# Kernel optimization log

Measured on AMD Instinct MI355X. Metric: run time of the kernel, lower is better.

Reference implementation:

```python
import jax, jax.numpy as jnp
import numpy as np

B, SI, ST, C, H, D = 1, 1024, 256, 3072, 24, 128
MLP = 4 * C
EPS = 1e-6
SCALE = 1.0 / float(np.sqrt(D))


def _ln(x):
    m = jnp.mean(x, -1, keepdims=True)
    v = jnp.var(x, -1, keepdims=True)
    return (x - m) / jnp.sqrt(v + EPS)


def _rms(x, w):
    return x * jax.lax.rsqrt(jnp.mean(x * x, -1, keepdims=True) + EPS) * w


def _mod(x, shift, scale):
    # AdaLN modulation: x * (1 + scale) + shift, scale/shift are [B, C]
    return x * (1.0 + scale[:, None, :]) + shift[:, None, :]


def _rot_half(x):
    xr, xi = x[..., 0::2], x[..., 1::2]
    return jnp.stack([-xi, xr], -1).reshape(x.shape)


def _rope(x, cos, sin):
    # x: [B, S, H, D]; cos/sin: [S, D]
    return x * cos[None, :, None, :] + _rot_half(x) * sin[None, :, None, :]


def _forward(img, txt, vec, fc, fs,
             i_mod_w, i_mod_b, i_qkv_w, i_qkv_b, i_qn, i_kn, i_pw, i_pb, i_f1w, i_f1b, i_f2w, i_f2b,
             t_mod_w, t_mod_b, t_qkv_w, t_qkv_b, t_qn, t_kn, t_pw, t_pb, t_f1w, t_f1b, t_f2w, t_f2b):
    sv = jax.nn.silu(vec)
    i_s1, i_c1, i_g1, i_s2, i_c2, i_g2 = jnp.split(sv @ i_mod_w + i_mod_b, 6, -1)
    t_s1, t_c1, t_g1, t_s2, t_c2, t_g2 = jnp.split(sv @ t_mod_w + t_mod_b, 6, -1)

    # img stream: LN -> modulate -> QKV -> qk RMSNorm -> RoPE
    iqkv = (_mod(_ln(img), i_s1, i_c1) @ i_qkv_w + i_qkv_b).reshape(B, SI, 3, H, D)
    iq = _rope(_rms(iqkv[:, :, 0], i_qn), fc, fs)
    ik = _rope(_rms(iqkv[:, :, 1], i_kn), fc, fs)
    iv = iqkv[:, :, 2]

    # txt stream: no RoPE
    tqkv = (_mod(_ln(txt), t_s1, t_c1) @ t_qkv_w + t_qkv_b).reshape(B, ST, 3, H, D)
    tq = _rms(tqkv[:, :, 0], t_qn)
    tk = _rms(tqkv[:, :, 1], t_kn)
    tv = tqkv[:, :, 2]

    q = jnp.concatenate([iq, tq], 1)
    k = jnp.concatenate([ik, tk], 1)
    v = jnp.concatenate([iv, tv], 1)

    logits = jnp.einsum('bqhd,bkhd->bhqk', q, k) * SCALE
    o = jnp.einsum('bhqk,bkhd->bqhd', jax.nn.softmax(logits, -1), v).reshape(B, SI + ST, C)
    ia, ta = o[:, :SI], o[:, SI:]

    img = img + (ia @ i_pw + i_pb) * i_g1[:, None, :]
    h = jax.nn.gelu(_mod(_ln(img), i_s2, i_c2) @ i_f1w + i_f1b, approximate=True)
    img = img + (h @ i_f2w + i_f2b) * i_g2[:, None, :]

    txt = txt + (ta @ t_pw + t_pb) * t_g1[:, None, :]
    h = jax.nn.gelu(_mod(_ln(txt), t_s2, t_c2) @ t_f1w + t_f1b, approximate=True)
    txt = txt + (h @ t_f2w + t_f2b) * t_g2[:, None, :]
    return img, txt


def setup_inputs() -> dict:
    key = jax.random.key(0)
    ki = iter(jax.random.split(key, 32))

    def w(shape, s=0.02):
        return jax.random.normal(next(ki), shape, jnp.float32) * s

    # RoPE tables shaped (img_seq_len, head_dim), interleaved pair layout
    pos = jnp.arange(SI, dtype=jnp.float32)
    inv = 1.0 / (10000.0 ** (jnp.arange(0, D, 2, dtype=jnp.float32) / D))
    ang = pos[:, None] * inv[None, :]
    inp = dict(
        img=jax.random.normal(next(ki), (B, SI, C), jnp.float32),
        txt=jax.random.normal(next(ki), (B, ST, C), jnp.float32),
        vec=jax.random.normal(next(ki), (B, C), jnp.float32),
        freqs_cos=jnp.repeat(jnp.cos(ang), 2, -1),
        freqs_sin=jnp.repeat(jnp.sin(ang), 2, -1),
    )
    for p in ('i', 't'):
        inp[p + '_mod_w'] = w((C, 6 * C)); inp[p + '_mod_b'] = jnp.zeros((6 * C,), jnp.float32)
        inp[p + '_qkv_w'] = w((C, 3 * C)); inp[p + '_qkv_b'] = jnp.zeros((3 * C,), jnp.float32)
        inp[p + '_qn'] = jnp.ones((D,), jnp.float32); inp[p + '_kn'] = jnp.ones((D,), jnp.float32)
        inp[p + '_pw'] = w((C, C)); inp[p + '_pb'] = jnp.zeros((C,), jnp.float32)
        inp[p + '_f1w'] = w((C, MLP)); inp[p + '_f1b'] = jnp.zeros((MLP,), jnp.float32)
        inp[p + '_f2w'] = w((MLP, C)); inp[p + '_f2b'] = jnp.zeros((C,), jnp.float32)
    return inp


def reference(img, txt, vec, freqs_cos, freqs_sin,
              i_mod_w, i_mod_b, i_qkv_w, i_qkv_b, i_qn, i_kn, i_pw, i_pb, i_f1w, i_f1b, i_f2w, i_f2b,
              t_mod_w, t_mod_b, t_qkv_w, t_qkv_b, t_qn, t_kn, t_pw, t_pb, t_f1w, t_f1b, t_f2w, t_f2b):
    return _forward(img, txt, vec, freqs_cos, freqs_sin,
                    i_mod_w, i_mod_b, i_qkv_w, i_qkv_b, i_qn, i_kn, i_pw, i_pb, i_f1w, i_f1b, i_f2w, i_f2b,
                    t_mod_w, t_mod_b, t_qkv_w, t_qkv_b, t_qn, t_kn, t_pw, t_pb, t_f1w, t_f1b, t_f2w, t_f2b)
```

## Files before the change

### kernel.cpp

```cpp
#include <hip/hip_runtime.h>


#define SI 1024
#define ST 256
#define SS 1280
#define CC 3072
#define NH 24
#define DH 128
#define MLPD 12288
#define EPSF 1e-6f
#define SCALEF 0.08838834764831845f

typedef __attribute__((ext_vector_type(4))) float f32x4;
typedef __attribute__((ext_vector_type(8))) __bf16 bf16x8;
typedef unsigned short u16;
typedef unsigned int u32;

__device__ __forceinline__ u16 f2bf(float x) {
    union { float f; u32 u; } v; v.f = x;
    u32 r = v.u + 0x7FFFu + ((v.u >> 16) & 1u);
    return (u16)(r >> 16);
}

__device__ __forceinline__ int gsw(int r) {
    return ((r >> 2) & 7) ^ ((r & 3) << 1);
}

__global__ __launch_bounds__(256) void k_modvec(
    const float* __restrict__ vec,
    const float* __restrict__ wi, const float* __restrict__ bi,
    const float* __restrict__ wt, const float* __restrict__ bt,
    float* __restrict__ mi, float* __restrict__ mt)
{
    __shared__ float sv[CC];
    __shared__ float part[7][128];
    int t = threadIdx.x;
    for (int i = t; i < CC; i += 256) {
        float x = vec[i];
        sv[i] = x / (1.f + __expf(-x));
    }
    __syncthreads();
    int gc = blockIdx.x;
    int strm = gc >= 144;
    const float* W  = strm ? wt : wi;
    const float* Bv = strm ? bt : bi;
    float* out      = strm ? mt : mi;
    int c0 = (gc % 144) * 128 + 4 * (t & 31);
    int g  = t >> 5;
    const float* wp  = W + (size_t)(g * 384) * (6 * CC) + c0;
    const float* svp = sv + g * 384;
    f32x4 acc = {0.f, 0.f, 0.f, 0.f};
    for (int r = 0; r < 384; ++r) {
        f32x4 wr = *(const f32x4*)(wp + (size_t)r * (6 * CC));
        float s = svp[r];
        acc.x += wr.x * s; acc.y += wr.y * s; acc.z += wr.z * s; acc.w += wr.w * s;
    }
    int li = t & 31;
    if (g > 0) *(f32x4*)&part[g - 1][li * 4] = acc;
    __syncthreads();
    if (g == 0) {
#pragma unroll
        for (int i = 0; i < 7; ++i) {
            f32x4 p = *(const f32x4*)&part[i][li * 4];
            acc.x += p.x; acc.y += p.y; acc.z += p.z; acc.w += p.w;
        }
        f32x4 bb = *(const f32x4*)(Bv + c0);
        acc.x += bb.x; acc.y += bb.y; acc.z += bb.z; acc.w += bb.w;
        *(f32x4*)(out + c0) = acc;
    }
}

__global__ __launch_bounds__(256) void k_lnmod(
    const float* __restrict__ x,
    const float* __restrict__ shift, const float* __restrict__ scale,
    u16* __restrict__ out)
{
    int r = blockIdx.x;
    const float* xp = x + (size_t)r * CC;
    u16* op = out + (size_t)r * CC;
    int t = threadIdx.x;
    float4 v[3];
    float s = 0.f, q = 0.f;
#pragma unroll
    for (int j = 0; j < 3; ++j) {
        v[j] = *(const float4*)(xp + j * 1024 + t * 4);
        s += v[j].x + v[j].y + v[j].z + v[j].w;
        q += v[j].x * v[j].x + v[j].y * v[j].y + v[j].z * v[j].z + v[j].w * v[j].w;
    }
#pragma unroll
    for (int m = 32; m; m >>= 1) { s += __shfl_xor(s, m); q += __shfl_xor(q, m); }
    __shared__ float red[8];
    int w = t >> 6;
    if ((t & 63) == 0) { red[w] = s; red[4 + w] = q; }
    __syncthreads();
    s = red[0] + red[1] + red[2] + red[3];
    q = red[4] + red[5] + red[6] + red[7];
    float mean = s * (1.f / CC);
    float var  = q * (1.f / CC) - mean * mean;
    float inv  = rsqrtf(var + EPSF);
#pragma unroll
    for (int j = 0; j < 3; ++j) {
        int c0 = j * 1024 + t * 4;
        float4 sh = *(const float4*)(shift + c0);
        float4 sc = *(const float4*)(scale + c0);
        ushort4 o;
        o.x = f2bf((v[j].x - mean) * inv * (1.f + sc.x) + sh.x);
        o.y = f2bf((v[j].y - mean) * inv * (1.f + sc.y) + sh.y);
        o.z = f2bf((v[j].z - mean) * inv * (1.f + sc.z) + sh.z);
        o.w = f2bf((v[j].w - mean) * inv * (1.f + sc.w) + sh.w);
        *(ushort4*)(op + c0) = o;
    }
}

template <int V, int BN>
__global__ __launch_bounds__(512, 2) void k_gemm(
    const u16* __restrict__ A,
    const float* __restrict__ Wi, const float* __restrict__ Wt,
    const float* __restrict__ bi, const float* __restrict__ bt,
    void* __restrict__ outv, int MBI, int N, int K, int lda)
{
    constexpr int BM  = 256;
    constexpr int NWN = (BN == 256) ? 4 : 2;
    constexpr int WM  = (BN == 256) ? 128 : 64;
    constexpr int MI  = WM / 16;
    constexpr int NFB = (BN == 256) ? 8 : 4;

    __shared__ u16 lA[2][BM * 64];
    __shared__ u16 lB[2][BN * 64];
    int t = threadIdx.x;
    int m0 = blockIdx.y * BM;
    int n0 = blockIdx.x * BN;
    bool txts = (blockIdx.y >= (unsigned)MBI);
    const float* W = txts ? Wt : Wi;
    const size_t koff = (size_t)blockIdx.z * K;

    int w = __builtin_amdgcn_readfirstlane(t >> 6);
    int lane = t & 63;
    int wm = (w / NWN) * WM, wn = (w % NWN) * 64;
    int lr = lane & 15, lg = lane >> 4;

    f32x4 acc[MI][4];
#pragma unroll
    for (int i = 0; i < MI; ++i)
#pragma unroll
        for (int j = 0; j < 4; ++j) acc[i][j] = (f32x4){0.f, 0.f, 0.f, 0.f};

    const int bn4 = (BN == 256) ? 4 * (t & 63) : 4 * (t & 31);
    const int bk  = (BN == 256) ? 8 * w : 4 * (t >> 5);
    f32x4 fb[NFB];
    const int NT = K >> 6;

    const float* bptr = W + (koff + bk) * (size_t)N + n0 + bn4;
    const int arow = t >> 3;
    const int acsw = ((t & 7) ^ gsw(arow)) * 8;
    const u16* aptr = A + (size_t)(m0 + arow) * lda + koff + acsw;

    auto LOADB = [&]() {
#pragma unroll
        for (int i = 0; i < NFB; ++i)
            fb[i] = *(const f32x4*)(bptr + (size_t)i * N);
        bptr += (size_t)64 * N;
    };
    auto GLDSA = [&](int buf) {
#pragma unroll
        for (int i = 0; i < 4; ++i) {
            const u16* gp = aptr + (size_t)(i * 64) * lda;
            u16* lp = &lA[buf][(i * 512 + t) * 8];
            __builtin_amdgcn_global_load_lds(
                (const __attribute__((address_space(1))) void*)gp,
                (__attribute__((address_space(3))) void*)lp, 16, 0, 0);
        }
        aptr += 64;
    };
    auto CVTWR = [&](int buf) {
        if constexpr (BN == 256) {
#pragma unroll
            for (int j = 0; j < 4; ++j) {
                int n = bn4 + j;
                union { uint4 q; __bf16 h[8]; } u;
#pragma unroll
                for (int i = 0; i < 8; ++i) u.h[i] = (__bf16)fb[i][j];
                int cp = (bk >> 3) ^ gsw(n);
                *(uint4*)&lB[buf][n * 64 + cp * 8] = u.q;
            }
        } else {
#pragma unroll
            for (int j = 0; j < 4; ++j) {
                int n = bn4 + j;
                union { uint2 q; __bf16 h[4]; } u;
#pragma unroll
                for (int i = 0; i < 4; ++i) u.h[i] = (__bf16)fb[i][j];
                int cp = (bk >> 3) ^ gsw(n);
                *(uint2*)&lB[buf][n * 64 + cp * 8 + (bk & 4)] = u.q;
            }
        }
    };
    auto MFMAP = [&](int buf) {
#pragma unroll
        for (int ks = 0; ks < 2; ++ks) {
            bf16x8 bv[4];
#pragma unroll
            for (int j = 0; j < 4; ++j) {
                int n = wn + j * 16 + lr;
                bv[j] = *(const bf16x8*)&lB[buf][n * 64 + (((ks * 4 + lg) ^ gsw(n)) * 8)];
            }
#pragma unroll
            for (int mh = 0; mh < MI / 4; ++mh) {
                bf16x8 af[4];
#pragma unroll
                for (int i2 = 0; i2 < 4; ++i2) {
                    int m = wm + (mh * 4 + i2) * 16 + lr;
                    af[i2] = *(const bf16x8*)&lA[buf][m * 64 + (((ks * 4 + lg) ^ gsw(m)) * 8)];
                }
                __builtin_amdgcn_s_setprio(1);
#pragma unroll
                for (int i2 = 0; i2 < 4; ++i2)
#pragma unroll
                    for (int j = 0; j < 4; ++j)
                        acc[mh * 4 + i2][j] = __builtin_amdgcn_mfma_f32_16x16x32_bf16(
                            af[i2], bv[j], acc[mh * 4 + i2][j], 0, 0, 0);
                __builtin_amdgcn_s_setprio(0);
            }
        }
    };
    auto VMWN = [&]() {
        if constexpr (BN == 256)
            asm volatile("s_waitcnt vmcnt(8) lgkmcnt(0)" ::: "memory");
        else
            asm volatile("s_waitcnt vmcnt(4) lgkmcnt(0)" ::: "memory");
    };

    LOADB();
    GLDSA(0);
    CVTWR(0);
    if (NT > 1) LOADB();
    VMWN();
    __builtin_amdgcn_s_barrier();
    __builtin_amdgcn_sched_barrier(0);

    int cur = 0;
    for (int kt = 0; kt < NT; ++kt) {
        bool s1 = kt + 1 < NT;
        bool s2 = kt + 2 < NT;
        if (s1) {
            GLDSA(cur ^ 1);
            CVTWR(cur ^ 1);
        }
        if (s2) LOADB();
        MFMAP(cur);
        if (s1) {
            if (s2) { VMWN(); }
            else    { asm volatile("s_waitcnt vmcnt(0) lgkmcnt(0)" ::: "memory"); }
            __builtin_amdgcn_s_barrier();
            __builtin_amdgcn_sched_barrier(0);
        }
        cur ^= 1;
    }

    const float* Bb = txts ? bt : bi;
    int MT = gridDim.y * BM;
#pragma unroll
    for (int i = 0; i < MI; ++i) {
#pragma unroll
        for (int j = 0; j < 4; ++j) {
            int col = n0 + wn + j * 16 + lr;
            float bvv = (V == 3) ? 0.f : Bb[col];
#pragma unroll
            for (int e = 0; e < 4; ++e) {
                int row = m0 + wm + i * 16 + lg * 4 + e;
                float val = acc[i][j][e] + bvv;
                if (V == 0) {
                    ((float*)outv)[(size_t)row * N + col] = val;
                } else if (V == 1) {
                    float g = 0.5f * val * (1.f + tanhf(0.7978845608028654f * (val + 0.044715f * val * val * val)));
                    ((u16*)outv)[(size_t)row * N + col] = f2bf(g);
                } else {
                    ((float*)outv)[((size_t)blockIdx.z * MT + row) * N + col] = val;
                }
            }
        }
    }
}

__global__ __launch_bounds__(256) void k_red(
    const float* __restrict__ p,
    const float* __restrict__ bi, const float* __restrict__ bt,
    const float* __restrict__ gi, const float* __restrict__ gt,
    const float* __restrict__ basei, const float* __restrict__ baset,
    float* __restrict__ out)
{
    int idx4 = blockIdx.x * 256 + threadIdx.x;
    size_t idx = (size_t)idx4 * 4;
    const size_t MN = (size_t)SS * CC;
    int r = idx4 / 768;
    int c = (idx4 - r * 768) * 4;
    bool ts = r >= SI;
    float4 v0 = *(const float4*)(p + idx);
    float4 v1 = *(const float4*)(p + MN + idx);
    float4 bb = *(const float4*)((ts ? bt : bi) + c);
    float4 gg = *(const float4*)((ts ? gt : gi) + c);
    const float* bp = ts ? (baset + (size_t)(r - SI) * CC + c) : (basei + (size_t)r * CC + c);
    float4 ba = *(const float4*)bp;
    float4 o;
    o.x = ba.x + (v0.x + v1.x + bb.x) * gg.x;
    o.y = ba.y + (v0.y + v1.y + bb.y) * gg.y;
    o.z = ba.z + (v0.z + v1.z + bb.z) * gg.z;
    o.w = ba.w + (v0.w + v1.w + bb.w) * gg.w;
    *(float4*)(out + idx) = o;
}

__global__ __launch_bounds__(256) void k_redln(
    const float* __restrict__ p,
    const float* __restrict__ bi, const float* __restrict__ bt,
    const float* __restrict__ gi, const float* __restrict__ gt,
    const float* __restrict__ basei, const float* __restrict__ baset,
    const float* __restrict__ shi, const float* __restrict__ sci,
    const float* __restrict__ sht, const float* __restrict__ sct,
    float* __restrict__ out, u16* __restrict__ xm)
{
    int r = blockIdx.x;
    int t = threadIdx.x;
    bool ts = r >= SI;
    const size_t MN = (size_t)SS * CC;
    const float* b  = ts ? bt : bi;
    const float* g  = ts ? gt : gi;
    const float* base = ts ? (baset + (size_t)(r - SI) * CC) : (basei + (size_t)r * CC);
    const float* p0 = p + (size_t)r * CC;
    const float* p1 = p0 + MN;
    float* op = out + (size_t)r * CC;
    u16*   xp = xm + (size_t)r * CC;

    float4 v[3];
    float s = 0.f, q = 0.f;
#pragma unroll
    for (int j = 0; j < 3; ++j) {
        int c0 = j * 1024 + t * 4;
        float4 a0 = *(const float4*)(p0 + c0);
        float4 a1 = *(const float4*)(p1 + c0);
        float4 bb = *(const float4*)(b + c0);
        float4 gg = *(const float4*)(g + c0);
        float4 ba = *(const float4*)(base + c0);
        float4 o;
        o.x = ba.x + (a0.x + a1.x + bb.x) * gg.x;
        o.y = ba.y + (a0.y + a1.y + bb.y) * gg.y;
        o.z = ba.z + (a0.z + a1.z + bb.z) * gg.z;
        o.w = ba.w + (a0.w + a1.w + bb.w) * gg.w;
        *(float4*)(op + c0) = o;
        v[j] = o;
        s += o.x + o.y + o.z + o.w;
        q += o.x * o.x + o.y * o.y + o.z * o.z + o.w * o.w;
    }
#pragma unroll
    for (int m = 32; m; m >>= 1) { s += __shfl_xor(s, m); q += __shfl_xor(q, m); }
    __shared__ float red[8];
    int w = t >> 6;
    if ((t & 63) == 0) { red[w] = s; red[4 + w] = q; }
    __syncthreads();
    s = red[0] + red[1] + red[2] + red[3];
    q = red[4] + red[5] + red[6] + red[7];
    float mean = s * (1.f / CC);
    float var  = q * (1.f / CC) - mean * mean;
    float inv  = rsqrtf(var + EPSF);
    const float* sh = ts ? sht : shi;
    const float* sc = ts ? sct : sci;
#pragma unroll
    for (int j = 0; j < 3; ++j) {
        int c0 = j * 1024 + t * 4;
        float4 shv = *(const float4*)(sh + c0);
        float4 scv = *(const float4*)(sc + c0);
        ushort4 o;
        o.x = f2bf((v[j].x - mean) * inv * (1.f + scv.x) + shv.x);
        o.y = f2bf((v[j].y - mean) * inv * (1.f + scv.y) + shv.y);
        o.z = f2bf((v[j].z - mean) * inv * (1.f + scv.z) + shv.z);
        o.w = f2bf((v[j].w - mean) * inv * (1.f + scv.w) + shv.w);
        *(ushort4*)(xp + c0) = o;
    }
}

__global__ __launch_bounds__(256) void k_pack(
    const float* __restrict__ qkv,
    const float* __restrict__ iqn, const float* __restrict__ ikn,
    const float* __restrict__ tqn, const float* __restrict__ tkn,
    const float* __restrict__ fc, const float* __restrict__ fs,
    u16* __restrict__ qpk, u16* __restrict__ kpk, u16* __restrict__ vpk)
{
    int wid = blockIdx.x * 4 + (threadIdx.x >> 6);
    int lane = threadIdx.x & 63;
    int s = wid / 72;
    int wh = wid % 72;
    int which = wh / 24;
    int h = wh % 24;
    int d = lane * 2;
    const float* src = qkv + (size_t)s * 9216 + which * 3072 + h * 128 + d;
    float x0 = src[0], x1 = src[1];
    float y0 = x0, y1 = x1;
    if (which < 2) {
        float ssq = x0 * x0 + x1 * x1;
#pragma unroll
        for (int m = 32; m; m >>= 1) ssq += __shfl_xor(ssq, m);
        float inv = rsqrtf(ssq * (1.f / 128.f) + EPSF);
        bool isimg = (s < SI);
        const float* wv = (which == 0) ? (isimg ? iqn : tqn) : (isimg ? ikn : tkn);
        y0 = x0 * inv * wv[d];
        y1 = x1 * inv * wv[d + 1];
        if (isimg) {
            float c0 = fc[s * 128 + d], c1 = fc[s * 128 + d + 1];
            float s0 = fs[s * 128 + d], s1 = fs[s * 128 + d + 1];
            float r0 = y0 * c0 - y1 * s0;
            float r1 = y1 * c1 + y0 * s1;
            y0 = r0; y1 = r1;
        }
        if (which == 0) { y0 *= SCALEF; y1 *= SCALEF; }
    }
    u16* dst = (which == 0) ? qpk : (which == 1) ? kpk : vpk;
    ushort2 o; o.x = f2bf(y0); o.y = f2bf(y1);
    *(ushort2*)(dst + ((size_t)h * SS + s) * 128 + d) = o;
}

__global__ __launch_bounds__(512, 1) void k_attn(
    const u16* __restrict__ qpk, const u16* __restrict__ kpk,
    const u16* __restrict__ vpk, u16* __restrict__ o)
{
    __shared__ u16 lK[128 * 136];
    __shared__ u16 lV[128 * 136];
    __shared__ u16 lP[128 * 136];
    int h = blockIdx.y;
    int q0 = blockIdx.x * 128;
    int t = threadIdx.x, w = t >> 6, lane = t & 63;
    int lr = lane & 15, lg = lane >> 4;
    const u16* qh = qpk + (size_t)h * SS * 128;
    const u16* kh = kpk + (size_t)h * SS * 128;
    const u16* vh = vpk + (size_t)h * SS * 128;

    bf16x8 aq[4];
#pragma unroll
    for (int kk = 0; kk < 4; ++kk)
        aq[kk] = *(const bf16x8*)(qh + (size_t)(q0 + w * 16 + lr) * 128 + kk * 32 + lg * 8);

    const f32x4 fz = {0.f, 0.f, 0.f, 0.f};
    f32x4 oa[8];
#pragma unroll
    for (int j = 0; j < 8; ++j) oa[j] = fz;
    float mrow[4], lrow[4];
#pragma unroll
    for (int e = 0; e < 4; ++e) { mrow[e] = -1e30f; lrow[e] = 0.f; }

    for (int kt = 0; kt < 10; ++kt) {
        int t0 = kt * 128;
        __syncthreads();
#pragma unroll
        for (int it = 0; it < 4; ++it) {
            int c = it * 512 + t;
            int row = c >> 4, part = c & 15;
            uint4 d4 = *(const uint4*)(kh + (size_t)(t0 + row) * 128 + part * 8);
            *(uint4*)(&lK[row * 136 + part * 8]) = d4;
        }
#pragma unroll
        for (int it = 0; it < 2; ++it) {
            int c = it * 512 + t;
            int pr = c >> 4;
            int tt = pr * 2;
            int k = c & 15;
            int d0 = k * 8;
            uint4 a = *(const uint4*)(vh + (size_t)(t0 + tt) * 128 + d0);
            uint4 b = *(const uint4*)(vh + (size_t)(t0 + tt + 1) * 128 + d0);
            const u16* a16 = (const u16*)&a;
            const u16* b16 = (const u16*)&b;
            int ts = tt ^ ((k & 7) << 3);
#pragma unroll
            for (int j = 0; j < 8; ++j) {
                ushort2 pv; pv.x = a16[j]; pv.y = b16[j];
                *(ushort2*)(&lV[(d0 + j) * 136 + ts]) = pv;
            }
        }
        __syncthreads();
        f32x4 sa[8];
#pragma unroll
        for (int j = 0; j < 8; ++j) sa[j] = fz;
#pragma unroll
        for (int kk = 0; kk < 4; ++kk) {
            bf16x8 bk[8];
#pragma unroll
            for (int ni = 0; ni < 8; ++ni)
                bk[ni] = *(const bf16x8*)(&lK[(ni * 16 + lr) * 136 + kk * 32 + lg * 8]);
#pragma unroll
            for (int ni = 0; ni < 8; ++ni)
                sa[ni] = __builtin_amdgcn_mfma_f32_16x16x32_bf16(aq[kk], bk[ni], sa[ni], 0, 0, 0);
        }
#pragma unroll
        for (int e = 0; e < 4; ++e) {
            float mx = sa[0][e];
#pragma unroll
            for (int ni = 1; ni < 8; ++ni) mx = fmaxf(mx, sa[ni][e]);
#pragma unroll
            for (int msk = 1; msk < 16; msk <<= 1) mx = fmaxf(mx, __shfl_xor(mx, msk));
            float mnew = fmaxf(mrow[e], mx);
            float esc = __expf(mrow[e] - mnew);
            mrow[e] = mnew;
            float rsum = 0.f;
#pragma unroll
            for (int ni = 0; ni < 8; ++ni) {
                float p = __expf(sa[ni][e] - mnew);
                sa[ni][e] = p;
                rsum += p;
            }
#pragma unroll
            for (int msk = 1; msk < 16; msk <<= 1) rsum += __shfl_xor(rsum, msk);
            lrow[e] = lrow[e] * esc + rsum;
#pragma unroll
            for (int nd = 0; nd < 8; ++nd) oa[nd][e] *= esc;
        }
#pragma unroll
        for (int ni = 0; ni < 8; ++ni)
#pragma unroll
            for (int e = 0; e < 4; ++e)
                lP[(w * 16 + lg * 4 + e) * 136 + ni * 16 + lr] = f2bf(sa[ni][e]);
#pragma unroll
        for (int kk = 0; kk < 4; ++kk) {
            bf16x8 pa, vb[8];
            pa = *(const bf16x8*)(&lP[(w * 16 + lr) * 136 + kk * 32 + lg * 8]);
#pragma unroll
            for (int nd = 0; nd < 8; ++nd) {
                int d = nd * 16 + lr;
                int ch = (kk * 4 + lg) ^ ((d >> 3) & 7);
                vb[nd] = *(const bf16x8*)(&lV[d * 136 + ch * 8]);
            }
#pragma unroll
            for (int nd = 0; nd < 8; ++nd)
                oa[nd] = __builtin_amdgcn_mfma_f32_16x16x32_bf16(pa, vb[nd], oa[nd], 0, 0, 0);
        }
    }
#pragma unroll
    for (int nd = 0; nd < 8; ++nd) {
#pragma unroll
        for (int e = 0; e < 4; ++e) {
            int row = q0 + w * 16 + lg * 4 + e;
            int col = h * 128 + nd * 16 + lr;
            o[(size_t)row * CC + col] = f2bf(oa[nd][e] / lrow[e]);
        }
    }
}

extern "C" void kernel_launch(void* const* d_in, const int* in_sizes, int n_in,
                              void* d_out, int out_size, void* d_ws, size_t ws_size,
                              hipStream_t stream)
{
    const float* img  = (const float*)d_in[0];
    const float* txt  = (const float*)d_in[1];
    const float* vec  = (const float*)d_in[2];
    const float* fc   = (const float*)d_in[3];
    const float* fs   = (const float*)d_in[4];
    const float* i_mod_w = (const float*)d_in[5];
    const float* i_mod_b = (const float*)d_in[6];
    const float* i_qkv_w = (const float*)d_in[7];
    const float* i_qkv_b = (const float*)d_in[8];
    const float* i_qn  = (const float*)d_in[9];
    const float* i_kn  = (const float*)d_in[10];
    const float* i_pw  = (const float*)d_in[11];
    const float* i_pb  = (const float*)d_in[12];
    const float* i_f1w = (const float*)d_in[13];
    const float* i_f1b = (const float*)d_in[14];
    const float* i_f2w = (const float*)d_in[15];
    const float* i_f2b = (const float*)d_in[16];
    const float* t_mod_w = (const float*)d_in[17];
    const float* t_mod_b = (const float*)d_in[18];
    const float* t_qkv_w = (const float*)d_in[19];
    const float* t_qkv_b = (const float*)d_in[20];
    const float* t_qn  = (const float*)d_in[21];
    const float* t_kn  = (const float*)d_in[22];
    const float* t_pw  = (const float*)d_in[23];
    const float* t_pb  = (const float*)d_in[24];
    const float* t_f1w = (const float*)d_in[25];
    const float* t_f1b = (const float*)d_in[26];
    const float* t_f2w = (const float*)d_in[27];
    const float* t_f2b = (const float*)d_in[28];

    char* ws = (char*)d_ws;
    float* mod_i = (float*)(ws + 0);
    float* mod_t = (float*)(ws + 73728);
    u16*   xmod  = (u16*)(ws + 147456);
    float* qkv   = (float*)(ws + 8011776);
    u16*   qpk   = (u16*)(ws + 55197696);
    u16*   kpk   = (u16*)(ws + 63062016);
    u16*   vpk   = (u16*)(ws + 70926336);
    u16*   obuf  = (u16*)(ws + 78790656);
    u16*   hbuf  = (u16*)(ws + 8011776);
    float* pbufP = (float*)(ws + 8011776);
    float* pbufF = (float*)(ws + 39469056);

    float* out_img = (float*)d_out;
    float* out_txt = out_img + (size_t)SI * CC;

    k_modvec<<<288, 256, 0, stream>>>(vec, i_mod_w, i_mod_b, t_mod_w, t_mod_b, mod_i, mod_t);

    k_lnmod<<<SI, 256, 0, stream>>>(img, mod_i + 0, mod_i + 3072, xmod);
    k_lnmod<<<ST, 256, 0, stream>>>(txt, mod_t + 0, mod_t + 3072, xmod + (size_t)SI * CC);

    k_gemm<0, 256><<<dim3(36, 5, 1), 512, 0, stream>>>(xmod, i_qkv_w, t_qkv_w, i_qkv_b, t_qkv_b,
                                                       qkv, 4, 9216, CC, CC);

    k_pack<<<23040, 256, 0, stream>>>(qkv, i_qn, i_kn, t_qn, t_kn, fc, fs, qpk, kpk, vpk);

    k_attn<<<dim3(10, 24), 512, 0, stream>>>(qpk, kpk, vpk, obuf);

    k_gemm<3, 128><<<dim3(24, 5, 2), 512, 0, stream>>>(obuf, i_pw, t_pw, nullptr, nullptr,
                                                       pbufP, 4, CC, CC / 2, CC);
    k_redln<<<SS, 256, 0, stream>>>(pbufP, i_pb, t_pb, mod_i + 6144, mod_t + 6144,
                                    img, txt,
                                    mod_i + 9216, mod_i + 12288,
                                    mod_t + 9216, mod_t + 12288,
                                    out_img, xmod);

    k_gemm<1, 256><<<dim3(48, 5, 1), 512, 0, stream>>>(xmod, i_f1w, t_f1w, i_f1b, t_f1b,
                                                       hbuf, 4, MLPD, CC, CC);

    k_gemm<3, 128><<<dim3(24, 5, 2), 512, 0, stream>>>(hbuf, i_f2w, t_f2w, nullptr, nullptr,
                                                       pbufF, 4, CC, MLPD / 2, MLPD);
    k_red<<<3840, 256, 0, stream>>>(pbufF, i_f2b, t_f2b, mod_i + 15360, mod_t + 15360,
                                    out_img, out_txt, out_img);
}
```

Before: 650.1 us.

## Store QKV GEMM output in bf16, merge LN launches, raise MFMA priority in attention

The QKV GEMM now writes bf16 instead of fp32, and the pack kernel reads bf16, which halves the traffic for the largest intermediate. The two LN-modulate launches are merged into one grid covering both the image and text rows. The attention kernel wraps its MFMA bursts in s_setprio so the matrix instructions get issue priority. Rounding QKV to bf16 before RMSNorm and RoPE adds a small precision loss.

```diff
diff --git a/kernel.cpp b/kernel.cpp
--- a/kernel.cpp
+++ b/kernel.cpp
@@ -20,6 +20,9 @@
     union { float f; u32 u; } v; v.f = x;
     u32 r = v.u + 0x7FFFu + ((v.u >> 16) & 1u);
     return (u16)(r >> 16);
+}
+__device__ __forceinline__ float bf2f(u16 x) {
+    union { u32 u; float f; } v; v.u = ((u32)x) << 16; return v.f;
 }
 
 __device__ __forceinline__ int gsw(int r) {
@@ -71,12 +74,16 @@
 }
 
 __global__ __launch_bounds__(256) void k_lnmod(
-    const float* __restrict__ x,
-    const float* __restrict__ shift, const float* __restrict__ scale,
+    const float* __restrict__ xi, const float* __restrict__ xt,
+    const float* __restrict__ shi, const float* __restrict__ sci,
+    const float* __restrict__ sht, const float* __restrict__ sct,
     u16* __restrict__ out)
 {
     int r = blockIdx.x;
-    const float* xp = x + (size_t)r * CC;
+    bool ts = r >= SI;
+    const float* xp = ts ? (xt + (size_t)(r - SI) * CC) : (xi + (size_t)r * CC);
+    const float* shift = ts ? sht : shi;
+    const float* scale = ts ? sct : sci;
     u16* op = out + (size_t)r * CC;
     int t = threadIdx.x;
     float4 v[3];
@@ -274,6 +281,8 @@
                 } else if (V == 1) {
                     float g = 0.5f * val * (1.f + tanhf(0.7978845608028654f * (val + 0.044715f * val * val * val)));
                     ((u16*)outv)[(size_t)row * N + col] = f2bf(g);
+                } else if (V == 2) {
+                    ((u16*)outv)[(size_t)row * N + col] = f2bf(val);
                 } else {
                     ((float*)outv)[((size_t)blockIdx.z * MT + row) * N + col] = val;
                 }
@@ -378,7 +387,7 @@
 }
 
 __global__ __launch_bounds__(256) void k_pack(
-    const float* __restrict__ qkv,
+    const u16* __restrict__ qkv,
     const float* __restrict__ iqn, const float* __restrict__ ikn,
     const float* __restrict__ tqn, const float* __restrict__ tkn,
     const float* __restrict__ fc, const float* __restrict__ fs,
@@ -391,8 +400,9 @@
     int which = wh / 24;
     int h = wh % 24;
     int d = lane * 2;
-    const float* src = qkv + (size_t)s * 9216 + which * 3072 + h * 128 + d;
-    float x0 = src[0], x1 = src[1];
+    const u16* src = qkv + (size_t)s * 9216 + which * 3072 + h * 128 + d;
+    ushort2 xv = *(const ushort2*)src;
+    float x0 = bf2f(xv.x), x1 = bf2f(xv.y);
     float y0 = x0, y1 = x1;
     if (which < 2) {
         float ssq = x0 * x0 + x1 * x1;
@@ -483,9 +493,11 @@
 #pragma unroll
             for (int ni = 0; ni < 8; ++ni)
                 bk[ni] = *(const bf16x8*)(&lK[(ni * 16 + lr) * 136 + kk * 32 + lg * 8]);
+            __builtin_amdgcn_s_setprio(1);
 #pragma unroll
             for (int ni = 0; ni < 8; ++ni)
                 sa[ni] = __builtin_amdgcn_mfma_f32_16x16x32_bf16(aq[kk], bk[ni], sa[ni], 0, 0, 0);
+            __builtin_amdgcn_s_setprio(0);
         }
 #pragma unroll
         for (int e = 0; e < 4; ++e) {
@@ -525,9 +537,11 @@
                 int ch = (kk * 4 + lg) ^ ((d >> 3) & 7);
                 vb[nd] = *(const bf16x8*)(&lV[d * 136 + ch * 8]);
             }
+            __builtin_amdgcn_s_setprio(1);
 #pragma unroll
             for (int nd = 0; nd < 8; ++nd)
                 oa[nd] = __builtin_amdgcn_mfma_f32_16x16x32_bf16(pa, vb[nd], oa[nd], 0, 0, 0);
+            __builtin_amdgcn_s_setprio(0);
         }
     }
 #pragma unroll
@@ -579,7 +593,7 @@
     float* mod_i = (float*)(ws + 0);
     float* mod_t = (float*)(ws + 73728);
     u16*   xmod  = (u16*)(ws + 147456);
-    float* qkv   = (float*)(ws + 8011776);
+    u16*   qkvb  = (u16*)(ws + 8011776);
     u16*   qpk   = (u16*)(ws + 55197696);
     u16*   kpk   = (u16*)(ws + 63062016);
     u16*   vpk   = (u16*)(ws + 70926336);
@@ -593,13 +607,13 @@
 
     k_modvec<<<288, 256, 0, stream>>>(vec, i_mod_w, i_mod_b, t_mod_w, t_mod_b, mod_i, mod_t);
 
-    k_lnmod<<<SI, 256, 0, stream>>>(img, mod_i + 0, mod_i + 3072, xmod);
-    k_lnmod<<<ST, 256, 0, stream>>>(txt, mod_t + 0, mod_t + 3072, xmod + (size_t)SI * CC);
-
-    k_gemm<0, 256><<<dim3(36, 5, 1), 512, 0, stream>>>(xmod, i_qkv_w, t_qkv_w, i_qkv_b, t_qkv_b,
-                                                       qkv, 4, 9216, CC, CC);
-
-    k_pack<<<23040, 256, 0, stream>>>(qkv, i_qn, i_kn, t_qn, t_kn, fc, fs, qpk, kpk, vpk);
+    k_lnmod<<<SS, 256, 0, stream>>>(img, txt, mod_i + 0, mod_i + 3072,
+                                    mod_t + 0, mod_t + 3072, xmod);
+
+    k_gemm<2, 256><<<dim3(36, 5, 1), 512, 0, stream>>>(xmod, i_qkv_w, t_qkv_w, i_qkv_b, t_qkv_b,
+                                                       qkvb, 4, 9216, CC, CC);
+
+    k_pack<<<23040, 256, 0, stream>>>(qkvb, i_qn, i_kn, t_qn, t_kn, fc, fs, qpk, kpk, vpk);
 
     k_attn<<<dim3(10, 24), 512, 0, stream>>>(qpk, kpk, vpk, obuf);
 
```

New measurement: 646.1 us (median of 2 runs). About the same (-0.6%).
